# Kernel optimization log

Hardware: AMD Instinct MI355X
Metric: run time of the kernel (lower is better)

The kernel has to match this reference:

```python
import jax, jax.numpy as jnp
import numpy as np

# static config (matches init_kwargs / input_specs)
LENS = (2048, 1024, 512, 256)   # per-level temporal lengths, sum = 3840
N, LQ, D_MODEL = 8, 2048, 256
M, L, P = 8, 4, 4               # heads, levels, points
D_HEAD = D_MODEL // M           # 32


def setup_inputs() -> dict:
    key = jax.random.key(0)
    ks = jax.random.split(key, 8)
    s = 0.02  # xavier-ish scale for 256-wide linears
    return {
        "query": jax.random.normal(ks[0], (N, LQ, D_MODEL), jnp.float32),
        "reference_points": jax.random.uniform(ks[1], (N, LQ, L, 1), dtype=jnp.float32),
        "input_flatten": jax.random.normal(ks[2], (N, sum(LENS), D_MODEL), jnp.float32),
        "input_temporal_lens": jnp.array(LENS, jnp.int32),
        "input_level_start_index": jnp.array(np.concatenate([[0], np.cumsum(LENS)[:-1]]), jnp.int32),
        "W_val": jax.random.normal(ks[3], (D_MODEL, D_MODEL), jnp.float32) * s,
        "b_val": jnp.zeros((D_MODEL,), jnp.float32),
        "W_off": jax.random.normal(ks[4], (M * L * P, D_MODEL), jnp.float32) * s,
        "b_off": jax.random.normal(ks[5], (M * L * P,), jnp.float32),  # mimics linspace bias init
        "W_attn": jax.random.normal(ks[6], (M * L * P, D_MODEL), jnp.float32) * s,
        "b_attn": jnp.zeros((M * L * P,), jnp.float32),
    }


def _sample_level(v, x, T):
    """1D bilinear sampling with zero padding, matching F.grid_sample
    (mode='bilinear', padding_mode='zeros', align_corners=False) on a (1,T) map.
    v: (N, T, M, D) level values; x: (N, Lq, M, P) normalized locations in [0,1].
    Returns (N, Lq, M, P, D)."""
    n, lq, m, p = x.shape
    ix = x * T - 0.5
    ix0 = jnp.floor(ix)
    w1 = (ix - ix0)[..., None]            # (N,Lq,M,P,1)
    i0 = ix0.astype(jnp.int32)

    def gather(idx):
        valid = ((idx >= 0) & (idx < T)).astype(v.dtype)
        idxc = jnp.clip(idx, 0, T - 1)
        flat = idxc.transpose(0, 1, 3, 2).reshape(n, lq * p, m)       # (N, Lq*P, M)
        g = jnp.take_along_axis(v, flat[..., None], axis=1)           # (N, Lq*P, M, D)
        g = g * valid.transpose(0, 1, 3, 2).reshape(n, lq * p, m)[..., None]
        return g.reshape(n, lq, p, m, -1).transpose(0, 1, 3, 2, 4)    # (N,Lq,M,P,D)

    return gather(i0) * (1.0 - w1) + gather(i0 + 1) * w1


def _deform_core(value, lens, loc, attn):
    """value: (N, S, M, D); loc: (N,Lq,M,L,P,1); attn: (N,Lq,M,L,P) -> (N,Lq,M*D)"""
    out = 0.0
    start = 0
    for lid, T in enumerate(lens):
        v = value[:, start:start + T]
        start += T
        s = _sample_level(v, loc[:, :, :, lid, :, 0], T)              # (N,Lq,M,P,D)
        out = out + jnp.einsum('nqmpd,nqmp->nqmd', s, attn[:, :, :, lid])
    n, lq, m, d = out.shape
    return out.reshape(n, lq, m * d)


def reference(query, reference_points, input_flatten, input_temporal_lens,
              input_level_start_index, W_val, b_val, W_off, b_off, W_attn, b_attn):
    lens = LENS  # static per-level lengths (needed for static slicing)
    value = (input_flatten @ W_val.T + b_val).reshape(N, sum(lens), M, D_HEAD)
    offs = (query @ W_off.T + b_off).reshape(N, LQ, M, L, P, 1)
    attn = jax.nn.softmax((query @ W_attn.T + b_attn).reshape(N, LQ, M, L * P), axis=-1)
    attn = attn.reshape(N, LQ, M, L, P)
    # reference_points last dim == 1, offset_normalizer=None branch
    norm = jnp.asarray(lens, query.dtype)[None, None, None, :, None, None]
    loc = reference_points[:, :, None, :, None, :] + offs / norm      # (N,Lq,M,L,P,1)
    # fp32 path of the torch module returns the core output WITHOUT output_proj
    return _deform_core(value, lens, loc, attn)
```

## Files before the change

kernel.cpp:

```cpp
#include <hip/hip_runtime.h>
#include <hip/hip_bf16.h>
#include <cstddef>

namespace {

constexpr int NB    = 8;
constexpr int LQn   = 2048;
constexpr int DM    = 256;
constexpr int S_TOT = 3840;

typedef __attribute__((ext_vector_type(8))) short  short8;
typedef __attribute__((ext_vector_type(4))) float  f32x4;
typedef __attribute__((ext_vector_type(8))) _Float16 half8;
typedef __attribute__((ext_vector_type(4))) _Float16 half4;
typedef __attribute__((ext_vector_type(2))) _Float16 half2v;

union BF8 { __hip_bfloat162 h2[4]; short8 s8; };
__device__ inline short8 cvt8(const f32x4 a, const f32x4 b) {
  BF8 r;
  r.h2[0] = __float22bfloat162_rn(make_float2(a[0], a[1]));
  r.h2[1] = __float22bfloat162_rn(make_float2(a[2], a[3]));
  r.h2[2] = __float22bfloat162_rn(make_float2(b[0], b[1]));
  r.h2[3] = __float22bfloat162_rn(make_float2(b[2], b[3]));
  return r.s8;
}

union SMem {
  struct { short A[128 * 64]; short B[128 * 64]; } ab;
  _Float16 c[128 * 136];
};

__global__ __launch_bounds__(256, 3) void gemm_bf16_k(
    const float* __restrict__ A_val, const float* __restrict__ A_prj,
    const float* __restrict__ W_val, const float* __restrict__ b_val,
    const float* __restrict__ W_off, const float* __restrict__ b_off,
    const float* __restrict__ W_att, const float* __restrict__ b_att,
    _Float16* __restrict__ out_val, _Float16* __restrict__ out_prj)
{
  __shared__ SMem sm;
  short* As = sm.ab.A;
  short* Bs = sm.ab.B;

  const int tid  = threadIdx.x;
  const int lane = tid & 63;
  const int wid  = tid >> 6;
  const int wm   = wid >> 1;
  const int wn   = wid & 1;

  const int id = blockIdx.x;
  const float *A, *W, *bias;
  int r0, c0;
  bool isv;
  int vbatch = 0, vtrow0 = 0;
  if (id < 480) {
    const int x = id & 7;
    const int s = id >> 3;
    const int rb = x * 30 + (s >> 1);
    const int c  = s & 1;
    A = A_val; r0 = rb * 128; c0 = c * 128;
    W = W_val + (size_t)c0 * DM; bias = b_val + c0;
    isv = true; vbatch = x; vtrow0 = (s >> 1) * 128;
  } else {
    const int j = id - 480;
    const int x = j & 7;
    const int s = j >> 3;
    const int rb = x * 16 + (s >> 1);
    const int c  = s & 1;
    A = A_prj; r0 = rb * 128; c0 = c * 128;
    W = c ? W_att : W_off; bias = c ? b_att : b_off;
    isv = false;
  }

  f32x4 acc[4][4] = {};

  float bv[4];
  #pragma unroll
  for (int ni = 0; ni < 4; ++ni)
    bv[ni] = bias[wn * 64 + ni * 16 + (lane & 15)];

  f32x4 pa0[4], pa1[4];

  auto load_A = [&](int k0) {
    #pragma unroll
    for (int i = 0; i < 4; ++i) {
      const int ch  = tid + i * 256;
      const int row = ch >> 3;
      const int kg  = ch & 7;
      const size_t goff = (size_t)(r0 + row) * DM + k0 + kg * 8;
      pa0[i] = *reinterpret_cast<const f32x4*>(&A[goff]);
      pa1[i] = *reinterpret_cast<const f32x4*>(&A[goff + 4]);
    }
  };

  load_A(0);

  for (int k = 0; k < 4; ++k) {
    const int k0 = k * 64;
    #pragma unroll 2
    for (int i = 0; i < 4; ++i) {
      const int ch  = tid + i * 256;
      const int row = ch >> 3;
      const int kg  = ch & 7;
      const size_t woff = (size_t)row * DM + k0 + kg * 8;
      const f32x4 w0 = *reinterpret_cast<const f32x4*>(&W[woff]);
      const f32x4 w1 = *reinterpret_cast<const f32x4*>(&W[woff + 4]);
      const short8 sw = cvt8(w0, w1);
      const int byte = row * 128 + ((kg * 16) ^ ((row & 7) << 4));
      *reinterpret_cast<short8*>(reinterpret_cast<char*>(Bs) + byte) = sw;
    }
    #pragma unroll
    for (int i = 0; i < 4; ++i) {
      const int ch  = tid + i * 256;
      const int row = ch >> 3;
      const int kg  = ch & 7;
      const short8 sa = cvt8(pa0[i], pa1[i]);
      const int byte = row * 128 + ((kg * 16) ^ ((row & 7) << 4));
      *reinterpret_cast<short8*>(reinterpret_cast<char*>(As) + byte) = sa;
    }
    if (k < 3) load_A(k0 + 64);

    asm volatile("s_waitcnt lgkmcnt(0)" ::: "memory");
    __builtin_amdgcn_sched_barrier(0);
    __builtin_amdgcn_s_barrier();
    __builtin_amdgcn_sched_barrier(0);

    #pragma unroll
    for (int ks = 0; ks < 2; ++ks) {
      const int kb = (ks * 32 + (lane >> 4) * 8) * 2;
      short8 af[4], bf[4];
      #pragma unroll
      for (int mi = 0; mi < 4; ++mi) {
        const int row = wm * 64 + mi * 16 + (lane & 15);
        const int byte = row * 128 + (kb ^ ((row & 7) << 4));
        af[mi] = *reinterpret_cast<const short8*>(
            reinterpret_cast<const char*>(As) + byte);
      }
      #pragma unroll
      for (int ni = 0; ni < 4; ++ni) {
        const int col = wn * 64 + ni * 16 + (lane & 15);
        const int byte = col * 128 + (kb ^ ((col & 7) << 4));
        bf[ni] = *reinterpret_cast<const short8*>(
            reinterpret_cast<const char*>(Bs) + byte);
      }
      #pragma unroll
      for (int mi = 0; mi < 4; ++mi)
        #pragma unroll
        for (int ni = 0; ni < 4; ++ni)
          acc[mi][ni] = __builtin_amdgcn_mfma_f32_16x16x32_bf16(
              af[mi], bf[ni], acc[mi][ni], 0, 0, 0);
    }

    asm volatile("s_waitcnt lgkmcnt(0)" ::: "memory");
    __builtin_amdgcn_sched_barrier(0);
    __builtin_amdgcn_s_barrier();
    __builtin_amdgcn_sched_barrier(0);
  }

  #pragma unroll
  for (int mi = 0; mi < 4; ++mi) {
    const int row = wm * 64 + mi * 16 + (lane >> 4) * 4;
    #pragma unroll
    for (int ni = 0; ni < 4; ++ni) {
      const int col = wn * 64 + ni * 16 + (lane & 15);
      #pragma unroll
      for (int j = 0; j < 4; ++j)
        sm.c[(row + j) * 136 + col] = (_Float16)(acc[mi][ni][j] + bv[ni]);
    }
  }
  __syncthreads();

  if (isv) {
    const size_t base = (size_t)vbatch * 8 * S_TOT + vtrow0;
    #pragma unroll
    for (int i = 0; i < 8; ++i) {
      const int ch  = tid + i * 256;
      const int hl  = ch >> 9;
      const int row = (ch >> 2) & 127;
      const int c4  = ch & 3;
      const half8 v = *reinterpret_cast<const half8*>(
          &sm.c[row * 136 + hl * 32 + c4 * 8]);
      const int h = (c0 >> 5) + hl;
      _Float16* dst = out_val + (base + (size_t)h * S_TOT + row) * 32 + c4 * 8;
      *reinterpret_cast<half8*>(dst) = v;
    }
  } else {
    #pragma unroll
    for (int i = 0; i < 8; ++i) {
      const int ch  = tid + i * 256;
      const int row = ch >> 4;
      const int cc  = ch & 15;
      const half8 v = *reinterpret_cast<const half8*>(&sm.c[row * 136 + cc * 8]);
      *reinterpret_cast<half8*>(&out_prj[(size_t)(r0 + row) * DM + c0 + cc * 8]) = v;
    }
  }
}

__global__ __launch_bounds__(512) void sample_k(
    const _Float16* __restrict__ proj,
    const float* __restrict__ refp,
    const _Float16* __restrict__ value,
    float* __restrict__ out)
{
  __shared__ uint4 tap_s[8][136];

  const int d     = blockIdx.x;
  const int n     = d & 7;
  const int chunk = d >> 3;
  const int row0q = n * LQn + chunk * 8;
  const int t     = threadIdx.x;

  const int lens[4]   = {2048, 1024, 512, 256};
  const int starts[4] = {0, 2048, 3072, 3584};

  if (t < 256) {
    const int q   = t >> 5;
    const int m   = (t >> 2) & 7;
    const int sub = t & 3;
    const int j0  = m * 16 + sub * 4;
    const size_t prow = (size_t)(row0q + q) * DM;

    const half4 offv = *reinterpret_cast<const half4*>(&proj[prow + j0]);
    const half4 lgv  = *reinterpret_cast<const half4*>(&proj[prow + 128 + j0]);
    float lg[4], off[4];
    #pragma unroll
    for (int i = 0; i < 4; ++i) { lg[i] = (float)lgv[i]; off[i] = (float)offv[i]; }

    float mx = fmaxf(fmaxf(lg[0], lg[1]), fmaxf(lg[2], lg[3]));
    mx = fmaxf(mx, __shfl_xor(mx, 1));
    mx = fmaxf(mx, __shfl_xor(mx, 2));
    float e[4], s = 0.f;
    #pragma unroll
    for (int i = 0; i < 4; ++i) { e[i] = __expf(lg[i] - mx); s += e[i]; }
    s += __shfl_xor(s, 1);
    s += __shfl_xor(s, 2);
    const float inv = 1.f / s;

    const int   T  = lens[sub];
    const int   st = starts[sub];
    const float fT = (float)T;
    const float rf = refp[(size_t)(row0q + q) * 4 + sub];
    #pragma unroll
    for (int i = 0; i < 4; ++i) {
      const float a  = e[i] * inv;
      const float ix = fmaf(rf, fT, off[i] - 0.5f);
      const float fl = floorf(ix);
      const float w1 = ix - fl;
      const int   i0 = (int)fl;
      const int   i1 = i0 + 1;
      const float wa = (i0 >= 0 && i0 < T) ? a * (1.f - w1) : 0.f;
      const float wb = (i1 >= 0 && i1 < T) ? a * w1 : 0.f;
      const int   r0b = (st + min(max(i0, 0), T - 1)) * 64;
      const int   r1b = (st + min(max(i1, 0), T - 1)) * 64;
      union { half2v h; unsigned u; } pw;
      pw.h.x = (_Float16)wa; pw.h.y = (_Float16)wb;
      uint4 ent; ent.x = pw.u; ent.y = (unsigned)r0b; ent.z = (unsigned)r1b; ent.w = 0u;
      tap_s[q][m * 17 + sub * 4 + i] = ent;
    }
  }
  __syncthreads();

  const int q  = t >> 6;
  const int l  = t & 63;
  const int m  = l >> 3;
  const int dg = l & 3;
  const int th = (l >> 2) & 1;
  const char* vb = reinterpret_cast<const char*>(value) +
                   (size_t)(n * 8 + m) * S_TOT * 64 + dg * 16;

  uint4 e[8];
  #pragma unroll
  for (int i = 0; i < 8; ++i) e[i] = tap_s[q][m * 17 + th * 8 + i];

  float acc[8] = {};
  half8 v0[4], v1[4];
  #pragma unroll
  for (int i = 0; i < 4; ++i) {
    v0[i] = *reinterpret_cast<const half8*>(vb + e[i].y);
    v1[i] = *reinterpret_cast<const half8*>(vb + e[i].z);
  }
  #pragma unroll
  for (int i = 0; i < 8; ++i) {
    const int s = i & 3;
    union { unsigned u; half2v h; } pw; pw.u = e[i].x;
    const float wa = (float)pw.h.x;
    const float wb = (float)pw.h.y;
    const half8 a0 = v0[s];
    const half8 a1 = v1[s];
    if (i < 4) {
      v0[s] = *reinterpret_cast<const half8*>(vb + e[i + 4].y);
      v1[s] = *reinterpret_cast<const half8*>(vb + e[i + 4].z);
    }
    #pragma unroll
    for (int j = 0; j < 8; ++j)
      acc[j] = fmaf(wa, (float)a0[j], fmaf(wb, (float)a1[j], acc[j]));
  }

  #pragma unroll
  for (int j = 0; j < 8; ++j) acc[j] += __shfl_xor(acc[j], 4);

  if (th == 0) {
    float* op = &out[(size_t)(row0q + q) * DM + m * 32 + dg * 8];
    f32x4 o0 = {acc[0], acc[1], acc[2], acc[3]};
    f32x4 o1 = {acc[4], acc[5], acc[6], acc[7]};
    *reinterpret_cast<f32x4*>(op)     = o0;
    *reinterpret_cast<f32x4*>(op + 4) = o1;
  }
}

}

extern "C" void kernel_launch(void* const* d_in, const int* in_sizes, int n_in,
                              void* d_out, int out_size, void* d_ws, size_t ws_size,
                              hipStream_t stream) {
  const float* query  = (const float*)d_in[0];
  const float* refp   = (const float*)d_in[1];
  const float* inflat = (const float*)d_in[2];
  const float* W_val  = (const float*)d_in[5];
  const float* b_val  = (const float*)d_in[6];
  const float* W_off  = (const float*)d_in[7];
  const float* b_off  = (const float*)d_in[8];
  const float* W_attn = (const float*)d_in[9];
  const float* b_attn = (const float*)d_in[10];
  float* out = (float*)d_out;

  _Float16* value_h = (_Float16*)d_ws;
  _Float16* proj_h  = (_Float16*)((char*)d_ws +
                      (size_t)NB * S_TOT * DM * sizeof(_Float16));

  gemm_bf16_k<<<dim3(736), dim3(256), 0, stream>>>(
      inflat, query, W_val, b_val, W_off, b_off, W_attn, b_attn,
      value_h, proj_h);

  sample_k<<<dim3(NB * LQn / 8), dim3(512), 0, stream>>>(
      proj_h, refp, value_h, out);
}
```

Measured before the change: 42.02 us.

## Widen GEMM tile to full 256 output columns with 512 threads and BK=32

The projection GEMM now computes a 128x256 tile per block with 8 waves instead of 128x128 with 4 waves, halving the grid and reading each A row tile once instead of twice. The K step drops from 64 to 32, using a k-group-major LDS layout without XOR swizzle. The epilogue writes the two 128-column halves through shared memory in two passes. The aim is to cut redundant fp32 A loads and conversions, at the cost of more barriers per K and possible LDS bank conflicts from the unswizzled layout.

```diff
diff --git a/kernel.cpp b/kernel.cpp
--- a/kernel.cpp
+++ b/kernel.cpp
@@ -8,6 +8,7 @@
 constexpr int LQn   = 2048;
 constexpr int DM    = 256;
 constexpr int S_TOT = 3840;
+constexpr int BK    = 32;
 
 typedef __attribute__((ext_vector_type(8))) short  short8;
 typedef __attribute__((ext_vector_type(4))) float  f32x4;
@@ -26,11 +27,11 @@
 }
 
 union SMem {
-  struct { short A[128 * 64]; short B[128 * 64]; } ab;
+  struct { short A[4 * 128 * 8]; short B[4 * 256 * 8]; } ab;
   _Float16 c[128 * 136];
 };
 
-__global__ __launch_bounds__(256, 3) void gemm_bf16_k(
+__global__ __launch_bounds__(512, 4) void gemm_bf16_k(
     const float* __restrict__ A_val, const float* __restrict__ A_prj,
     const float* __restrict__ W_val, const float* __restrict__ b_val,
     const float* __restrict__ W_off, const float* __restrict__ b_off,
@@ -38,116 +39,106 @@
     _Float16* __restrict__ out_val, _Float16* __restrict__ out_prj)
 {
   __shared__ SMem sm;
-  short* As = sm.ab.A;
-  short* Bs = sm.ab.B;
+  char* As = reinterpret_cast<char*>(sm.ab.A);
+  char* Bs = reinterpret_cast<char*>(sm.ab.B);
 
   const int tid  = threadIdx.x;
   const int lane = tid & 63;
   const int wid  = tid >> 6;
-  const int wm   = wid >> 1;
-  const int wn   = wid & 1;
+  const int wm   = wid >> 2;
+  const int wn   = wid & 3;
 
   const int id = blockIdx.x;
-  const float *A, *W, *bias;
-  int r0, c0;
+  const float* A;
   bool isv;
-  int vbatch = 0, vtrow0 = 0;
-  if (id < 480) {
+  int r0, vbatch = 0, vtrow0 = 0;
+  if (id < 240) {
     const int x = id & 7;
     const int s = id >> 3;
-    const int rb = x * 30 + (s >> 1);
-    const int c  = s & 1;
-    A = A_val; r0 = rb * 128; c0 = c * 128;
-    W = W_val + (size_t)c0 * DM; bias = b_val + c0;
-    isv = true; vbatch = x; vtrow0 = (s >> 1) * 128;
+    A = A_val; r0 = (x * 30 + s) * 128;
+    isv = true; vbatch = x; vtrow0 = s * 128;
   } else {
-    const int j = id - 480;
+    const int j = id - 240;
     const int x = j & 7;
     const int s = j >> 3;
-    const int rb = x * 16 + (s >> 1);
-    const int c  = s & 1;
-    A = A_prj; r0 = rb * 128; c0 = c * 128;
-    W = c ? W_att : W_off; bias = c ? b_att : b_off;
+    A = A_prj; r0 = (x * 16 + s) * 128;
     isv = false;
   }
 
+  float bv[4];
+  #pragma unroll
+  for (int ni = 0; ni < 4; ++ni) {
+    const int col = wn * 64 + ni * 16 + (lane & 15);
+    bv[ni] = isv ? b_val[col]
+                 : (col < 128 ? b_off[col] : b_att[col - 128]);
+  }
+
+  const int arow = tid >> 2;
+  const int akg  = tid & 3;
+
+  const float* wrow0;
+  const float* wrow1;
+  if (isv) {
+    wrow0 = W_val + (size_t)arow * DM;
+    wrow1 = W_val + (size_t)(arow + 128) * DM;
+  } else {
+    wrow0 = W_off + (size_t)arow * DM;
+    wrow1 = W_att + (size_t)arow * DM;
+  }
+
+  f32x4 pa0, pa1;
+  auto load_A = [&](int k0) {
+    const float* p = &A[(size_t)(r0 + arow) * DM + k0 + akg * 8];
+    pa0 = *reinterpret_cast<const f32x4*>(p);
+    pa1 = *reinterpret_cast<const f32x4*>(p + 4);
+  };
+  load_A(0);
+
   f32x4 acc[4][4] = {};
 
-  float bv[4];
-  #pragma unroll
-  for (int ni = 0; ni < 4; ++ni)
-    bv[ni] = bias[wn * 64 + ni * 16 + (lane & 15)];
-
-  f32x4 pa0[4], pa1[4];
-
-  auto load_A = [&](int k0) {
-    #pragma unroll
-    for (int i = 0; i < 4; ++i) {
-      const int ch  = tid + i * 256;
-      const int row = ch >> 3;
-      const int kg  = ch & 7;
-      const size_t goff = (size_t)(r0 + row) * DM + k0 + kg * 8;
-      pa0[i] = *reinterpret_cast<const f32x4*>(&A[goff]);
-      pa1[i] = *reinterpret_cast<const f32x4*>(&A[goff + 4]);
-    }
-  };
-
-  load_A(0);
-
-  for (int k = 0; k < 4; ++k) {
-    const int k0 = k * 64;
-    #pragma unroll 2
-    for (int i = 0; i < 4; ++i) {
-      const int ch  = tid + i * 256;
-      const int row = ch >> 3;
-      const int kg  = ch & 7;
-      const size_t woff = (size_t)row * DM + k0 + kg * 8;
-      const f32x4 w0 = *reinterpret_cast<const f32x4*>(&W[woff]);
-      const f32x4 w1 = *reinterpret_cast<const f32x4*>(&W[woff + 4]);
-      const short8 sw = cvt8(w0, w1);
-      const int byte = row * 128 + ((kg * 16) ^ ((row & 7) << 4));
-      *reinterpret_cast<short8*>(reinterpret_cast<char*>(Bs) + byte) = sw;
-    }
-    #pragma unroll
-    for (int i = 0; i < 4; ++i) {
-      const int ch  = tid + i * 256;
-      const int row = ch >> 3;
-      const int kg  = ch & 7;
-      const short8 sa = cvt8(pa0[i], pa1[i]);
-      const int byte = row * 128 + ((kg * 16) ^ ((row & 7) << 4));
-      *reinterpret_cast<short8*>(reinterpret_cast<char*>(As) + byte) = sa;
-    }
-    if (k < 3) load_A(k0 + 64);
+  for (int k = 0; k < 8; ++k) {
+    const int k0 = k * BK;
+    {
+      const float* p0 = wrow0 + k0 + akg * 8;
+      const f32x4 w00 = *reinterpret_cast<const f32x4*>(p0);
+      const f32x4 w01 = *reinterpret_cast<const f32x4*>(p0 + 4);
+      const short8 sw0 = cvt8(w00, w01);
+      *reinterpret_cast<short8*>(Bs + akg * 4096 + arow * 16) = sw0;
+      const float* p1 = wrow1 + k0 + akg * 8;
+      const f32x4 w10 = *reinterpret_cast<const f32x4*>(p1);
+      const f32x4 w11 = *reinterpret_cast<const f32x4*>(p1 + 4);
+      const short8 sw1 = cvt8(w10, w11);
+      *reinterpret_cast<short8*>(Bs + akg * 4096 + (arow + 128) * 16) = sw1;
+    }
+    {
+      const short8 sa = cvt8(pa0, pa1);
+      *reinterpret_cast<short8*>(As + akg * 2048 + arow * 16) = sa;
+    }
+    if (k < 7) load_A(k0 + BK);
 
     asm volatile("s_waitcnt lgkmcnt(0)" ::: "memory");
     __builtin_amdgcn_sched_barrier(0);
     __builtin_amdgcn_s_barrier();
     __builtin_amdgcn_sched_barrier(0);
 
-    #pragma unroll
-    for (int ks = 0; ks < 2; ++ks) {
-      const int kb = (ks * 32 + (lane >> 4) * 8) * 2;
-      short8 af[4], bf[4];
+    {
+      const int kgl = lane >> 4;
+      const int rl  = lane & 15;
+      short8 af[4], bfr[4];
       #pragma unroll
-      for (int mi = 0; mi < 4; ++mi) {
-        const int row = wm * 64 + mi * 16 + (lane & 15);
-        const int byte = row * 128 + (kb ^ ((row & 7) << 4));
+      for (int mi = 0; mi < 4; ++mi)
         af[mi] = *reinterpret_cast<const short8*>(
-            reinterpret_cast<const char*>(As) + byte);
-      }
+            As + kgl * 2048 + (wm * 64 + mi * 16 + rl) * 16);
       #pragma unroll
-      for (int ni = 0; ni < 4; ++ni) {
-        const int col = wn * 64 + ni * 16 + (lane & 15);
-        const int byte = col * 128 + (kb ^ ((col & 7) << 4));
-        bf[ni] = *reinterpret_cast<const short8*>(
-            reinterpret_cast<const char*>(Bs) + byte);
-      }
+      for (int ni = 0; ni < 4; ++ni)
+        bfr[ni] = *reinterpret_cast<const short8*>(
+            Bs + kgl * 4096 + (wn * 64 + ni * 16 + rl) * 16);
       #pragma unroll
       for (int mi = 0; mi < 4; ++mi)
         #pragma unroll
         for (int ni = 0; ni < 4; ++ni)
           acc[mi][ni] = __builtin_amdgcn_mfma_f32_16x16x32_bf16(
-              af[mi], bf[ni], acc[mi][ni], 0, 0, 0);
+              af[mi], bfr[ni], acc[mi][ni], 0, 0, 0);
     }
 
     asm volatile("s_waitcnt lgkmcnt(0)" ::: "memory");
@@ -157,41 +148,38 @@
   }
 
   #pragma unroll
-  for (int mi = 0; mi < 4; ++mi) {
-    const int row = wm * 64 + mi * 16 + (lane >> 4) * 4;
-    #pragma unroll
-    for (int ni = 0; ni < 4; ++ni) {
-      const int col = wn * 64 + ni * 16 + (lane & 15);
+  for (int hh = 0; hh < 2; ++hh) {
+    if ((wn >> 1) == hh) {
       #pragma unroll
-      for (int j = 0; j < 4; ++j)
-        sm.c[(row + j) * 136 + col] = (_Float16)(acc[mi][ni][j] + bv[ni]);
-    }
-  }
-  __syncthreads();
-
-  if (isv) {
-    const size_t base = (size_t)vbatch * 8 * S_TOT + vtrow0;
-    #pragma unroll
-    for (int i = 0; i < 8; ++i) {
-      const int ch  = tid + i * 256;
-      const int hl  = ch >> 9;
-      const int row = (ch >> 2) & 127;
-      const int c4  = ch & 3;
-      const half8 v = *reinterpret_cast<const half8*>(
-          &sm.c[row * 136 + hl * 32 + c4 * 8]);
-      const int h = (c0 >> 5) + hl;
-      _Float16* dst = out_val + (base + (size_t)h * S_TOT + row) * 32 + c4 * 8;
-      *reinterpret_cast<half8*>(dst) = v;
-    }
-  } else {
-    #pragma unroll
-    for (int i = 0; i < 8; ++i) {
-      const int ch  = tid + i * 256;
+      for (int mi = 0; mi < 4; ++mi) {
+        const int row = wm * 64 + mi * 16 + (lane >> 4) * 4;
+        #pragma unroll
+        for (int ni = 0; ni < 4; ++ni) {
+          const int coll = (wn & 1) * 64 + ni * 16 + (lane & 15);
+          #pragma unroll
+          for (int j = 0; j < 4; ++j)
+            sm.c[(row + j) * 136 + coll] = (_Float16)(acc[mi][ni][j] + bv[ni]);
+        }
+      }
+    }
+    __syncthreads();
+    #pragma unroll
+    for (int i = 0; i < 4; ++i) {
+      const int ch  = tid + i * 512;
       const int row = ch >> 4;
       const int cc  = ch & 15;
       const half8 v = *reinterpret_cast<const half8*>(&sm.c[row * 136 + cc * 8]);
-      *reinterpret_cast<half8*>(&out_prj[(size_t)(r0 + row) * DM + c0 + cc * 8]) = v;
-    }
+      if (isv) {
+        const int h = hh * 4 + (cc >> 2);
+        _Float16* dst = out_val +
+            ((size_t)(vbatch * 8 + h) * S_TOT + vtrow0 + row) * 32 + (cc & 3) * 8;
+        *reinterpret_cast<half8*>(dst) = v;
+      } else {
+        *reinterpret_cast<half8*>(
+            &out_prj[(size_t)(r0 + row) * DM + hh * 128 + cc * 8]) = v;
+      }
+    }
+    __syncthreads();
   }
 }
 
@@ -327,7 +315,7 @@
   _Float16* proj_h  = (_Float16*)((char*)d_ws +
                       (size_t)NB * S_TOT * DM * sizeof(_Float16));
 
-  gemm_bf16_k<<<dim3(736), dim3(256), 0, stream>>>(
+  gemm_bf16_k<<<dim3(368), dim3(512), 0, stream>>>(
       inflat, query, W_val, b_val, W_off, b_off, W_attn, b_attn,
       value_h, proj_h);
 
```

New measurement: 42.11 us. No clear change (+0.2%).
